# Kernel tuning notes

Hardware: AMD Instinct MI355X
Metric: run time of the kernel (lower is better)

The kernel has to match this reference:

```python
import jax, jax.numpy as jnp
import numpy as np

B_IN, B_MID, B_OUT = 30, 16, 10   # band widths: input sphere, after S2 conv, after SO3 conv
F1, F2 = 100, 100                 # feature channels
EPS = 1e-5


def _qw(b):
    """Driscoll-Healy quadrature weights over the 2b beta samples (SOFT grid)."""
    j = np.arange(2 * b)
    k = np.arange(b)
    s = (np.sin(np.pi * (2 * j[:, None] + 1) * (2 * k[None, :] + 1) / (4 * b))
         / (2 * k[None, :] + 1)).sum(1)
    return ((2.0 / b) * np.sin(np.pi * (2 * j + 1) / (4 * b)) * s).astype(np.float32)


def _wigner_d_all(l_max, betas):
    """Wigner-d matrices d^l(beta) = exp(-i beta Jy) in the |l,m> basis (m = -l..l).
    Returns list over l of real arrays [n_beta, 2l+1, 2l+1]."""
    betas = np.asarray(betas, np.float64)
    out = []
    for l in range(l_max):
        m = np.arange(-l, l + 1)
        dim = 2 * l + 1
        Jp = np.zeros((dim, dim))
        for i in range(dim - 1):
            Jp[i + 1, i] = np.sqrt(l * (l + 1) - m[i] * (m[i] + 1))
        Jy = (Jp - Jp.T) / 2j
        ev, V = np.linalg.eigh(Jy)
        ph = np.exp(-1j * betas[:, None] * ev[None, :])
        d = np.einsum('ak,bk,ck->bac', V, ph, V.conj())
        out.append(np.real(d).astype(np.float32))
    return out


def _project(x, b):
    """Radial max-projection of a point cloud [B,3,N] onto a (beta,alpha) grid -> [B,1,2b,2b]."""
    r = jnp.sqrt(jnp.sum(x * x, axis=1) + 1e-12)                       # [B,N]
    beta = jnp.arccos(jnp.clip(x[:, 2] / r, -1 + 1e-7, 1 - 1e-7))      # [0,pi]
    alpha = jnp.mod(jnp.arctan2(x[:, 1], x[:, 0]), 2 * np.pi)          # [0,2pi)
    jb = jnp.clip((beta / np.pi * (2 * b)).astype(jnp.int32), 0, 2 * b - 1)
    ja = jnp.clip((alpha / (2 * np.pi) * (2 * b)).astype(jnp.int32), 0, 2 * b - 1)
    flat = jb * (2 * b) + ja
    img = jax.vmap(lambda f, v: jnp.zeros((2 * b) ** 2, x.dtype).at[f].max(v))(flat, r)
    return img.reshape(x.shape[0], 1, 2 * b, 2 * b)


def _s2_fft(x, dm0_w):
    """x: [B,F,2b,2b] (beta,alpha) -> list over l of x_hat [B,F,2l+1] (complex)."""
    X = jnp.fft.fft(x, axis=-1)     # FFT over alpha
    n = x.shape[-1]
    hats = []
    for l, dw in enumerate(dm0_w):
        idx = np.mod(np.arange(-l, l + 1), n)
        hats.append(jnp.einsum('pm,BFpm->BFm', jnp.asarray(dw), X[..., idx]))
    return hats


def _so3_fft(x, dmn_w):
    """x: [B,F,2b,2b,2b] (beta,alpha,gamma) -> list over l of [B,F,2l+1,2l+1]."""
    X = jnp.fft.fftn(x, axes=(-2, -1))   # FFT over alpha, gamma
    n = x.shape[-1]
    hats = []
    for l, dw in enumerate(dmn_w):
        idx = np.mod(np.arange(-l, l + 1), n)
        Xl = X[:, :, :, idx[:, None], idx[None, :]]        # [B,F,2b,2l+1,2l+1]
        hats.append(jnp.einsum('pmn,BFpmn->BFmn', jnp.asarray(dw), Xl))
    return hats


def _so3_ifft(hats, b, d_list):
    """list over l of [B,F,2l+1,2l+1] -> real SO(3) signal [B,F,2b,2b,2b]."""
    Bb, Ff = hats[0].shape[:2]
    n = 2 * b
    Fg = jnp.zeros((Bb, Ff, n, n, n), jnp.complex64)   # (beta, m, n) freq grid
    for l, h in enumerate(hats):
        idx = np.mod(np.arange(-l, l + 1), n)
        c = (2 * l + 1) * jnp.einsum('pmn,BFmn->BFpmn', jnp.asarray(d_list[l]), h)
        Fg = Fg.at[:, :, :, idx[:, None], idx[None, :]].add(c)
    return jnp.real(jnp.fft.ifft2(Fg, axes=(-2, -1)))


def _bn_relu(x, g, b):
    mu = jnp.mean(x, axis=(0, 2, 3, 4), keepdims=True)
    var = jnp.var(x, axis=(0, 2, 3, 4), keepdims=True)
    xn = (x - mu) * jax.lax.rsqrt(var + EPS)
    return jax.nn.relu(xn * g[None, :, None, None, None] + b[None, :, None, None, None])


def _forward(x, w_s2, b_s2, bn1_gamma, bn1_beta, w_so3, b_so3, bn2_gamma, bn2_beta):
    # constant tables (numpy, computed eagerly)
    betas_in = (np.arange(2 * B_IN) + 0.5) * np.pi / (2 * B_IN)
    betas_mid = (np.arange(2 * B_MID) + 0.5) * np.pi / (2 * B_MID)
    betas_out = (np.arange(2 * B_OUT) + 0.5) * np.pi / (2 * B_OUT)
    w_in, w_mid, w_out = _qw(B_IN), _qw(B_MID), _qw(B_OUT)
    d_in = _wigner_d_all(B_MID, betas_in)
    d_mid = _wigner_d_all(B_MID, betas_mid)
    d_out = _wigner_d_all(B_OUT, betas_out)
    d_eq = _wigner_d_all(B_MID, np.array([np.pi / 2]))   # equatorial grid beta = pi/2

    img = _project(x, B_IN)                              # [B,1,60,60]

    # ---- S2 convolution: band 30 -> 16 ----
    dm0_w = [d_in[l][:, :, l] * w_in[:, None] for l in range(B_MID)]   # d^l_{m0} * quad weights
    xhat = _s2_fft(img, dm0_w)                           # list of [B,1,2l+1]
    k_s2 = w_s2.shape[-1]
    a_s2 = 2 * np.pi * np.arange(k_s2) / k_s2
    ws = w_s2 * np.float32(1.0 / np.sqrt(k_s2 * 1 * B_MID ** 4 / B_IN ** 2))
    zhat = []
    for l in range(B_MID):
        m = np.arange(-l, l + 1)
        sh = (d_eq[l][0][:, l][None, :] * np.exp(-1j * np.outer(a_s2, m))).astype(np.complex64)  # [k,m]
        yh = jnp.einsum('km,iok->mio', jnp.asarray(sh), ws)           # kernel spectrum [2l+1,f_in,f_out]
        zhat.append(jnp.einsum('Bim,nio->Bomn', xhat[l], jnp.conj(yh)))  # outer product m x n
    z = _so3_ifft(zhat, B_MID, d_mid) + b_s2[None, :, None, None, None]  # [B,100,32,32,32]
    z = _bn_relu(z, bn1_gamma, bn1_beta)

    # ---- SO3 convolution: band 16 -> 10 ----
    dmn_w = [d_mid[l] * w_mid[:, None, None] for l in range(B_OUT)]
    xhat2 = _so3_fft(z, dmn_w)                           # list of [B,100,2l+1,2l+1]
    k_so3 = w_so3.shape[-1]
    a_so3 = 2 * np.pi * np.arange(k_so3) / k_so3
    wk = w_so3 * np.float32(1.0 / np.sqrt(k_so3 * F1 * B_OUT ** 3 / B_MID ** 3))
    zhat2 = []
    for l in range(B_OUT):
        m = np.arange(-l, l + 1)
        U = (d_eq[l][0][None] * np.exp(-1j * np.outer(a_so3, m))[:, :, None]).astype(np.complex64)  # [k,m,n], gamma=0
        yh = jnp.einsum('kmn,iok->mnio', jnp.asarray(U), wk)
        zhat2.append(jnp.einsum('Bimk,nkio->Bomn', xhat2[l], jnp.conj(yh)))  # z^l = x^l y^l+
    z2 = _so3_ifft(zhat2, B_OUT, d_out) + b_so3[None, :, None, None, None]   # [B,100,20,20,20]
    z2 = _bn_relu(z2, bn2_gamma, bn2_beta)

    # ---- so3_integrate: sum over alpha/gamma, quadrature-weighted sum over beta ----
    return jnp.einsum('BCpag,p->BC', z2, jnp.asarray(w_out))   # [B,100]


def setup_inputs() -> dict:
    key = jax.random.key(0)
    k0, k1, k2 = jax.random.split(key, 3)
    B, N = 8, 2048
    return {
        "x": jax.random.normal(k0, (B, 3, N), jnp.float32),
        "w_s2": jax.random.normal(k1, (1, F1, 2 * B_IN), jnp.float32),
        "b_s2": jnp.zeros((F1,), jnp.float32),
        "bn1_gamma": jnp.ones((F1,), jnp.float32),
        "bn1_beta": jnp.zeros((F1,), jnp.float32),
        "w_so3": jax.random.normal(k2, (F1, F2, 2 * B_MID), jnp.float32),
        "b_so3": jnp.zeros((F2,), jnp.float32),
        "bn2_gamma": jnp.ones((F2,), jnp.float32),
        "bn2_beta": jnp.zeros((F2,), jnp.float32),
    }


def reference(x, w_s2, b_s2, bn1_gamma, bn1_beta, w_so3, b_so3, bn2_gamma, bn2_beta):
    return _forward(x, w_s2, b_s2, bn1_gamma, bn1_beta, w_so3, b_so3, bn2_gamma, bn2_beta)
```

## Files before the change

kernel.cpp:

```cpp
#include <hip/hip_runtime.h>
#include <math.h>

#define PI_D 3.14159265358979323846

constexpr int NBATCH = 8;
constexpr int NPTS   = 2048;
constexpr int F1C    = 100;
constexpr int F2C    = 100;

__host__ __device__ constexpr int S2c(int l){ return l*(2*l-1)*(2*l+1)/3; }

constexpr int OFF_WIN   = 0;
constexpr int OFF_WMID  = OFF_WIN + 60;
constexpr int OFF_WOUTQ = OFF_WMID + 32;
constexpr int OFF_DM0W  = OFF_WOUTQ + 20;
constexpr int OFF_DMID  = OFF_DM0W + 60*256;
constexpr int OFF_DOUT  = OFF_DMID + 32*S2c(16);
constexpr int OFF_DEQ   = OFF_DOUT + 20*S2c(10);
constexpr int OFF_IMG   = OFF_DEQ + S2c(16);
constexpr int OFF_XF    = OFF_IMG + NBATCH*60*60;
constexpr int OFF_XHAT  = OFF_XF + NBATCH*60*31*2;
constexpr int OFF_WS2   = OFF_XHAT + NBATCH*256*2;
constexpr int OFF_BN1   = OFF_WS2 + 100*31*2;
constexpr int OFF_BN1AB = OFF_BN1 + 200;
constexpr int OFF_BN2   = OFF_BN1AB + 200;
constexpr int OFF_BN2AB = OFF_BN2 + 200;
constexpr int OFF_LUTA  = OFF_BN2AB + 200;
constexpr int OFF_LUTB  = OFF_LUTA + 1330;
constexpr int OFF_LUTC  = OFF_LUTB + 1330;
constexpr int OFF_WCONV = OFF_LUTC + 1330;
constexpr int OFF_XHAT2 = OFF_WCONV + 100*100*19*2;
constexpr int OFF_SBUF  = OFF_XHAT2 + NBATCH*100*S2c(10)*2;
constexpr int OFF_ZHAT2 = OFF_SBUF + NBATCH*100*S2c(10)*2;
constexpr int OFF_Z2    = OFF_ZHAT2 + NBATCH*100*S2c(10)*2;
constexpr int OFF_Z     = OFF_Z2 + NBATCH*100*20*20*20;
constexpr int WS_TOTAL  = OFF_Z + NBATCH*100*32*32*32;
constexpr int OFF_HBUF  = OFF_Z2;

__device__ __forceinline__ int S2d(int l){ return l*(2*l-1)*(2*l+1)/3; }

__global__ void k_quad(float* ws){
  int j = threadIdx.x;
  if (j < 60){
    double bb = 30.0, s = 0.0;
    for (int k = 0; k < 30; ++k) s += sin(PI_D*(2*j+1)*(2*k+1)/(4.0*bb))/(2*k+1);
    ws[OFF_WIN+j] = (float)(2.0/bb * sin(PI_D*(2*j+1)/(4.0*bb)) * s);
  }
  if (j < 32){
    double bb = 16.0, s = 0.0;
    for (int k = 0; k < 16; ++k) s += sin(PI_D*(2*j+1)*(2*k+1)/(4.0*bb))/(2*k+1);
    ws[OFF_WMID+j] = (float)(2.0/bb * sin(PI_D*(2*j+1)/(4.0*bb)) * s);
  }
  if (j < 20){
    double bb = 10.0, s = 0.0;
    for (int k = 0; k < 10; ++k) s += sin(PI_D*(2*j+1)*(2*k+1)/(4.0*bb))/(2*k+1);
    ws[OFF_WOUTQ+j] = (float)(2.0/bb * sin(PI_D*(2*j+1)/(4.0*bb)) * s);
  }
}

__global__ void k_lut(float* ws){
  int q = blockIdx.x*blockDim.x + threadIdx.x;
  if (q >= 1330) return;
  int l = 0; while (S2d(l+1) <= q) ++l;
  int loc = q - S2d(l), tl = 2*l+1;
  int mm = loc/tl, nn = loc%tl;
  ((int*)(ws+OFF_LUTA))[q] = 32*S2d(l) + mm*tl + nn;
  ((int*)(ws+OFF_LUTB))[q] = ((mm-l+9)*19 + (nn-l+9)) | ((tl*tl) << 9) | ((nn-l+9) << 19);
  ((int*)(ws+OFF_LUTC))[q] = (S2d(l) + mm*tl) | ((S2d(l) + nn*tl) << 11) | (tl << 22);
}

__device__ double dev_wigner_t(const double* fact, int l, int mp, int m, double beta){
  double ch = cos(0.5*beta), sh = sin(0.5*beta);
  int kmin = m - mp; if (kmin < 0) kmin = 0;
  int kmax = l + m; if (l - mp < kmax) kmax = l - mp;
  double pref = sqrt(fact[l+mp]*fact[l-mp]*fact[l+m]*fact[l-m]);
  int ec = 2*l + m - mp - 2*kmin, es = mp - m + 2*kmin;
  double cp = 1.0, sp = 1.0;
  for (int e = 0; e < ec; ++e) cp *= ch;
  for (int e = 0; e < es; ++e) sp *= sh;
  double ch2i = 1.0/(ch*ch), sh2 = sh*sh;
  double sum = 0.0;
  for (int k = kmin; k <= kmax; ++k){
    double t = 1.0/(fact[l+m-k]*fact[k]*fact[l-mp-k]*fact[mp-m+k]);
    if ((mp-m+k) & 1) t = -t;
    sum += t*cp*sp;
    cp *= ch2i; sp *= sh2;
  }
  return pref*sum;
}

constexpr int N_DM0W = 60*256;
constexpr int N_DMID = 32*S2c(16);
constexpr int N_DOUT = 20*S2c(10);
constexpr int N_DEQ  = S2c(16);
constexpr int N_WIG  = N_DM0W + N_DMID + N_DOUT + N_DEQ;

__global__ void k_wigner(float* ws){
  __shared__ double fact[32];
  if (threadIdx.x == 0){ fact[0] = 1.0; for (int i = 1; i < 32; ++i) fact[i] = fact[i-1]*i; }
  __syncthreads();
  int idx = blockIdx.x*blockDim.x + threadIdx.x;
  if (idx >= N_WIG) return;
  if (idx < N_DM0W){
    int l = 0; while (60*(l+1)*(l+1) <= idx) ++l;
    int rem = idx - 60*l*l, tl = 2*l+1;
    int p = rem/tl, mm = rem%tl;
    double beta = (p+0.5)*PI_D/60.0;
    ws[OFF_DM0W+idx] = (float)dev_wigner_t(fact, l, mm-l, 0, beta) * ws[OFF_WIN+p];
    return;
  }
  idx -= N_DM0W;
  if (idx < N_DMID){
    int l = 0; while (32*S2d(l+1) <= idx) ++l;
    int rem = idx - 32*S2d(l), tl = 2*l+1;
    int q = rem % (tl*tl), p = rem/(tl*tl);
    int mm = q/tl, nn = q%tl;
    double beta = (p+0.5)*PI_D/32.0;
    ws[OFF_DMID+idx] = (float)dev_wigner_t(fact, l, mm-l, nn-l, beta);
    return;
  }
  idx -= N_DMID;
  if (idx < N_DOUT){
    int l = 0; while (20*S2d(l+1) <= idx) ++l;
    int rem = idx - 20*S2d(l), tl = 2*l+1;
    int q = rem % (tl*tl), p = rem/(tl*tl);
    int mm = q/tl, nn = q%tl;
    double beta = (p+0.5)*PI_D/20.0;
    ws[OFF_DOUT+idx] = (float)dev_wigner_t(fact, l, mm-l, nn-l, beta);
    return;
  }
  idx -= N_DOUT;
  {
    int l = 0; while (S2d(l+1) <= idx) ++l;
    int rem = idx - S2d(l), tl = 2*l+1;
    int mm = rem/tl, nn = rem%tl;
    ws[OFF_DEQ+idx] = (float)dev_wigner_t(fact, l, mm-l, nn-l, 0.5*PI_D);
  }
}

__global__ void k_project(const float* __restrict__ x, float* ws){
  int t = blockIdx.x*blockDim.x + threadIdx.x;
  if (t >= NBATCH*NPTS) return;
  int b = t / NPTS, n = t % NPTS;
  const float* xb = x + (size_t)b*3*NPTS;
  float xx = xb[n], yy = xb[NPTS+n], zz = xb[2*NPTS+n];
  float r = sqrtf(xx*xx + yy*yy + zz*zz + 1e-12f);
  float ct = zz / r;
  ct = fminf(fmaxf(ct, -1.0f + 1e-7f), 1.0f - 1e-7f);
  float beta = acosf(ct);
  float alpha = atan2f(yy, xx);
  if (alpha < 0.0f) alpha += 2.0f*(float)PI_D;
  int jb = (int)((beta / (float)PI_D) * 60.0f);
  jb = jb < 0 ? 0 : (jb > 59 ? 59 : jb);
  int ja = (int)((alpha / (2.0f*(float)PI_D)) * 60.0f);
  ja = ja < 0 ? 0 : (ja > 59 ? 59 : ja);
  unsigned* img = (unsigned*)(ws + OFF_IMG) + (b*3600 + jb*60 + ja);
  atomicMax(img, __float_as_uint(r));
}

__global__ void k_s2dft(float* ws){
  int t = blockIdx.x*blockDim.x + threadIdx.x;
  if (t >= NBATCH*60*31) return;
  int b = t/(60*31), r = t%(60*31);
  int p = r/31, mi = r%31, m = mi - 15;
  const float* img = ws + OFF_IMG + (b*60 + p)*60;
  float sr = 0.f, si = 0.f;
  for (int a = 0; a < 60; ++a){
    int k = ((a*m) % 60 + 60) % 60;
    float c = cospif(k/30.0f), s = sinpif(k/30.0f);
    float v = img[a];
    sr += v*c; si -= v*s;
  }
  ws[OFF_XF + t*2]   = sr;
  ws[OFF_XF + t*2+1] = si;
}

__global__ void k_xhat(float* ws){
  int t = blockIdx.x*blockDim.x + threadIdx.x;
  if (t >= NBATCH*256) return;
  int b = t/256, flat = t%256;
  int l = 0; while ((l+1)*(l+1) <= flat) ++l;
  int mm = flat - l*l, tl = 2*l+1;
  int mi = mm - l + 15;
  float sr = 0.f, si = 0.f;
  for (int p = 0; p < 60; ++p){
    float w = ws[OFF_DM0W + 60*l*l + p*tl + mm];
    sr += w * ws[OFF_XF + ((b*60+p)*31 + mi)*2];
    si += w * ws[OFF_XF + ((b*60+p)*31 + mi)*2 + 1];
  }
  ws[OFF_XHAT + t*2]   = sr;
  ws[OFF_XHAT + t*2+1] = si;
}

__global__ void k_ws2(float* ws, const float* __restrict__ w_s2, float scale1){
  int t = blockIdx.x*blockDim.x + threadIdx.x;
  if (t >= 100*31) return;
  int o = t/31, ni = t%31, n = ni - 15;
  float sr = 0.f, si = 0.f;
  for (int k = 0; k < 60; ++k){
    int kk = ((k*n) % 60 + 60) % 60;
    float c = cospif(kk/30.0f), s = sinpif(kk/30.0f);
    float v = w_s2[o*60 + k] * scale1;
    sr += v*c; si += v*s;
  }
  ws[OFF_WS2 + t*2]   = sr;
  ws[OFF_WS2 + t*2+1] = si;
}

__global__ __launch_bounds__(256) void k_H(float* ws){
  int bid = blockIdx.x;
  int p = bid & 31, b = bid >> 5;
  __shared__ float xh[512], Dt[256];
  __shared__ int dbase[16];
  int tid = threadIdx.x;
  {
    int flat = tid;
    int l = 0; while ((l+1)*(l+1) <= flat) ++l;
    int mm = flat - l*l, tl = 2*l+1;
    xh[2*flat]   = ws[OFF_XHAT + (b*256+flat)*2];
    xh[2*flat+1] = ws[OFF_XHAT + (b*256+flat)*2+1];
    Dt[flat] = (float)tl * ws[OFF_DEQ + S2d(l) + mm*tl + l];
  }
  if (tid < 16){ int l = tid, tl = 2*l+1; dbase[l] = OFF_DMID + 32*S2d(l) + p*tl*tl; }
  __syncthreads();
  float* Hb = ws + OFF_HBUF + (size_t)bid*992;
  for (int q = tid; q < 496; q += 256){
    int m = q/31, ni = q%31, n = ni-15;
    int an = n < 0 ? -n : n;
    int lmin = m > an ? m : an;
    float ar = 0.f, ai = 0.f;
    for (int l = lmin; l < 16; ++l){
      int tl = 2*l+1;
      float d = ws[dbase[l] + (m+l)*tl + (n+l)];
      float t = d * Dt[l*l + (n+l)];
      int fa = l*l + (m+l);
      ar += t*xh[2*fa]; ai += t*xh[2*fa+1];
    }
    Hb[2*q] = ar; Hb[2*q+1] = ai;
  }
}

__global__ __launch_bounds__(256) void k_so3ifft_mid(float* ws, const float* __restrict__ b_s2){
  int bid = blockIdx.x;
  int p = bid & 31, bo = bid >> 5;
  int o = bo % F1C, b = bo / F1C;
  __shared__ float Fg[992], tmpS[1024];
  __shared__ float twr[32], twi[32], Wr[31], Wi[31], redA[4], redB[4];
  int tid = threadIdx.x;
  if (tid < 32){ twr[tid] = cospif(tid/16.0f); twi[tid] = sinpif(tid/16.0f); }
  if (tid < 31){ Wr[tid] = ws[OFF_WS2 + (o*31+tid)*2]; Wi[tid] = ws[OFF_WS2 + (o*31+tid)*2+1]; }
  __syncthreads();
  {
    const float* Hb = ws + OFF_HBUF + (size_t)((b<<5)|p)*992;
    for (int q = tid; q < 496; q += 256){
      int ni = q % 31;
      float hr = Hb[2*q], hi = Hb[2*q+1];
      float wr = Wr[ni], wi = Wi[ni];
      Fg[2*q]   = hr*wr - hi*wi;
      Fg[2*q+1] = hr*wi + hi*wr;
    }
  }
  __syncthreads();
  if (tid < 128){
    int m = tid >> 3, g0 = tid & 7;
    float T0r=0,T0i=0,T1r=0,T1i=0,T2r=0,T2i=0,T3r=0,T3i=0;
    int base = 2*m*31;
    #pragma unroll
    for (int ni = 0; ni < 31; ++ni){
      int k = ((ni-15)*g0) & 31;
      float c = twr[k], s = twi[k];
      float fr = Fg[base+2*ni], fi = Fg[base+2*ni+1];
      float re = fr*c - fi*s, im = fr*s + fi*c;
      int cc = (ni+1) & 3;
      if (cc == 0){ T0r += re; T0i += im; }
      else if (cc == 1){ T1r += re; T1i += im; }
      else if (cc == 2){ T2r += re; T2i += im; }
      else { T3r += re; T3i += im; }
    }
    float Ar=T0r+T2r, Ai=T0i+T2i, Br=T0r-T2r, Bi=T0i-T2i;
    float Cr=T1r+T3r, Ci=T1i+T3i, Dr=T1r-T3r, Di=T1i-T3i;
    int ix = 2*(m*32+g0);
    tmpS[ix]      = Ar+Cr; tmpS[ix+1]    = Ai+Ci;
    tmpS[ix+16]   = Br-Di; tmpS[ix+17]   = Bi+Dr;
    tmpS[ix+32]   = Ar-Cr; tmpS[ix+33]   = Ai-Ci;
    tmpS[ix+48]   = Br+Di; tmpS[ix+49]   = Bi-Dr;
  }
  __syncthreads();
  float bsv = b_s2[o];
  float lsum = 0.f, lss = 0.f;
  float* z = ws + OFF_Z;
  size_t zb = ((size_t)(b*F1C+o)*32 + p)*1024;
  {
    int a0 = tid >> 5, g = tid & 31;
    float U0r=0, U2r=0, U1r=0, U1i=0, U3r=0, U3i=0;
    #pragma unroll
    for (int m = 1; m < 16; ++m){
      int k = (m*a0) & 31;
      float c = twr[k], s = twi[k];
      float tr = tmpS[2*(m*32+g)], ti = tmpS[2*(m*32+g)+1];
      float re = tr*c - ti*s;
      int cc = m & 3;
      if (cc == 0) U0r += re;
      else if (cc == 2) U2r += re;
      else {
        float im = tr*s + ti*c;
        if (cc == 1){ U1r += re; U1i += im; }
        else        { U3r += re; U3i += im; }
      }
    }
    float Ar = U0r + U2r, Br = U0r - U2r;
    float Cr = U1r + U3r, Di = U1i - U3i;
    float t0 = tmpS[2*g];
    float v0 = (t0 + 2.0f*(Ar + Cr))*(1.0f/1024.0f) + bsv;
    float v1 = (t0 + 2.0f*(Br - Di))*(1.0f/1024.0f) + bsv;
    float v2 = (t0 + 2.0f*(Ar - Cr))*(1.0f/1024.0f) + bsv;
    float v3 = (t0 + 2.0f*(Br + Di))*(1.0f/1024.0f) + bsv;
    z[zb + (a0     )*32 + g] = v0;
    z[zb + (a0 +  8)*32 + g] = v1;
    z[zb + (a0 + 16)*32 + g] = v2;
    z[zb + (a0 + 24)*32 + g] = v3;
    lsum = v0+v1+v2+v3;
    lss  = v0*v0+v1*v1+v2*v2+v3*v3;
  }
  for (int off = 32; off; off >>= 1){ lsum += __shfl_down(lsum, off); lss += __shfl_down(lss, off); }
  if ((tid & 63) == 0){ redA[tid>>6] = lsum; redB[tid>>6] = lss; }
  __syncthreads();
  if (tid == 0){
    atomicAdd(&ws[OFF_BN1 + o],       redA[0]+redA[1]+redA[2]+redA[3]);
    atomicAdd(&ws[OFF_BN1 + 100 + o], redB[0]+redB[1]+redB[2]+redB[3]);
  }
}

__global__ void k_bnfin1(float* ws, const float* __restrict__ g1, const float* __restrict__ be1){
  int t = threadIdx.x;
  if (t >= 100) return;
  const float invN = 1.0f/262144.0f;
  float mu = ws[OFF_BN1+t]*invN;
  float var = ws[OFF_BN1+100+t]*invN - mu*mu;
  float sA = rsqrtf(var + 1e-5f) * g1[t];
  ws[OFF_BN1AB+t]     = sA;
  ws[OFF_BN1AB+100+t] = be1[t] - mu*sA;
}

__global__ __launch_bounds__(256) void k_so3fft_a(float* ws){
  int bid = blockIdx.x;
  int p = bid & 31, bo = bid >> 5;
  int o = bo % F1C;
  __shared__ float y[32*33];
  __shared__ float Bs[32*36];
  __shared__ float t1[1216];
  __shared__ float twr[32], twi[32];
  int tid = threadIdx.x;
  if (tid < 32){ twr[tid] = cospif(tid/16.0f); twi[tid] = sinpif(tid/16.0f); }
  float sA = ws[OFF_BN1AB+o], sB = ws[OFF_BN1AB+100+o];
  float* zp = ws + OFF_Z + (size_t)bid*1024;
  for (int q = tid; q < 1024; q += 256){
    float v = zp[q]*sA + sB;
    y[(q>>5)*33 + (q&31)] = v > 0.f ? v : 0.f;
  }
  __syncthreads();
  {
    int a = tid >> 3, g2 = tid & 7;
    float y0 = y[a*33+g2], y1 = y[a*33+g2+8], y2 = y[a*33+g2+16], y3 = y[a*33+g2+24];
    float e = y0+y2, f = y1+y3;
    int bb = a*36 + g2*4;
    Bs[bb]   = e+f;
    Bs[bb+1] = e-f;
    Bs[bb+2] = y0-y2;
    Bs[bb+3] = -(y1-y3);
  }
  __syncthreads();
  for (int q = tid; q < 320; q += 256){
    int a = q/10, n = q%10, ni = 9+n;
    int c = n & 3;
    int bb = a*36;
    float sr = 0.f, si = 0.f;
    if ((c & 1) == 0){
      int off = bb + (c >> 1);
      #pragma unroll
      for (int g2 = 0; g2 < 8; ++g2){
        int k = (g2*n) & 31;
        float B = Bs[off + g2*4];
        sr += B*twr[k]; si -= B*twi[k];
      }
    } else {
      float sgn = (c == 1) ? 1.f : -1.f;
      #pragma unroll
      for (int g2 = 0; g2 < 8; ++g2){
        int k = (g2*n) & 31;
        float cc_ = twr[k], ss = twi[k];
        float br = Bs[bb+g2*4+2], bi = sgn*Bs[bb+g2*4+3];
        sr += br*cc_ + bi*ss;
        si += bi*cc_ - br*ss;
      }
    }
    t1[2*(a*19+ni)] = sr; t1[2*(a*19+ni)+1] = si;
  }
  __syncthreads();
  for (int q = tid; q < 160; q += 256){
    int a = q/10, ni = 9 + q%10;
    int i0 = 2*(a*19+ni), i1 = 2*((a+16)*19+ni);
    float xr=t1[i0], xi=t1[i0+1], yr=t1[i1], yi=t1[i1+1];
    t1[i0]=xr+yr; t1[i0+1]=xi+yi; t1[i1]=xr-yr; t1[i1+1]=xi-yi;
  }
  __syncthreads();
  float wm = ws[OFF_WMID+p];
  for (int q = tid; q < 190; q += 256){
    int m = q/10 - 9, nio = q%10, ni = 9+nio;
    int off = (m & 1) ? 16*19 : 0;
    float sr = 0.f, si = 0.f;
    for (int a = 0; a < 16; ++a){
      int k = (a*m) & 31;
      float c = twr[k], s = twi[k];
      float tr = t1[2*(off+a*19+ni)], ti = t1[2*(off+a*19+ni)+1];
      sr += tr*c + ti*s;
      si += ti*c - tr*s;
    }
    sr *= wm; si *= wm;
    int qf = (m+9)*19 + ni;
    zp[2*qf] = sr; zp[2*qf+1] = si;
    if (nio > 0){
      int qm = (9-m)*19 + (9-nio);
      zp[2*qm] = sr; zp[2*qm+1] = -si;
    }
  }
}

__global__ __launch_bounds__(512) void k_so3fft_b(float* ws){
  int bo = blockIdx.x;
  int tid = threadIdx.x;
  __shared__ float xw[722];
  __shared__ float xh2[2660];
  const float* xwbase = ws + OFF_Z + (size_t)bo*32*1024;
  const int* lutA = (const int*)(ws + OFF_LUTA);
  const int* lutB = (const int*)(ws + OFF_LUTB);
  const int* lutC = (const int*)(ws + OFF_LUTC);
  float accr[3], acci[3];
  int la[3], xi2[3], tl2v[3];
  #pragma unroll
  for (int j = 0; j < 3; ++j){
    accr[j] = 0.f; acci[j] = 0.f;
    int q = tid + 512*j;
    if (q < 1330){ la[j] = lutA[q]; int lb = lutB[q]; xi2[j] = 2*(lb & 511); tl2v[j] = (lb >> 9) & 1023; }
    else { la[j] = 0; xi2[j] = 0; tl2v[j] = 0; }
  }
  for (int pp = 0; pp < 32; ++pp){
    __syncthreads();
    for (int u = tid; u < 722; u += 512) xw[u] = xwbase[pp*1024 + u];
    __syncthreads();
    #pragma unroll
    for (int j = 0; j < 3; ++j){
      int q = tid + 512*j;
      if (q < 1330){
        float d = ws[OFF_DMID + la[j] + pp*tl2v[j]];
        accr[j] += d*xw[xi2[j]]; acci[j] += d*xw[xi2[j]+1];
      }
    }
  }
  #pragma unroll
  for (int j = 0; j < 3; ++j){
    int q = tid + 512*j;
    if (q < 1330){ xh2[2*q] = accr[j]; xh2[2*q+1] = acci[j]; }
  }
  __syncthreads();
  #pragma unroll
  for (int j = 0; j < 3; ++j){
    int q = tid + 512*j;
    if (q < 1330){
      int lc = lutC[q];
      int rowstart = lc & 2047, deqrow = (lc >> 11) & 2047, tl = lc >> 22;
      const float* dq = ws + OFF_DEQ + deqrow;
      const float* xb = xh2 + 2*rowstart;
      float sr = 0.f, si = 0.f;
      for (int k = 0; k < tl; ++k){
        float d = dq[k];
        sr += d*xb[2*k]; si += d*xb[2*k+1];
      }
      int base = OFF_SBUF + (bo*1330 + q)*2;
      ws[base]   = sr;
      ws[base+1] = si;
    }
  }
}

__global__ void k_wconv(float* ws, const float* __restrict__ w_so3, float scale2){
  int t = blockIdx.x*blockDim.x + threadIdx.x;
  if (t >= 100*100*19) return;
  int ni = t % 19, io = t / 19;
  int n = ni - 9;
  float sr = 0.f, si = 0.f;
  for (int j = 0; j < 32; ++j){
    int k = (j*n) & 31;
    float c = cospif(k/16.0f), s = sinpif(k/16.0f);
    float v = w_so3[io*32 + j] * scale2;
    sr += v*c; si += v*s;
  }
  ws[OFF_WCONV + t*2]   = sr;
  ws[OFF_WCONV + t*2+1] = si;
}

__global__ void k_zhat2(float* ws){
  int t = blockIdx.x*blockDim.x + threadIdx.x;
  if (t >= NBATCH*50*1330) return;
  int q = t % 1330, boo = t / 1330;
  int oq = boo % 50, b = boo / 50;
  int o0 = oq*2;
  int lb = ((const int*)(ws+OFF_LUTB))[q];
  int ni = (lb >> 19) & 31;
  const float* sp  = ws + OFF_SBUF + (size_t)(b*100)*2660 + 2*q;
  const float* wp0 = ws + OFF_WCONV + (size_t)(o0*19 + ni)*2;
  const float* wp1 = wp0 + 38;
  float sr0 = 0.f, si0 = 0.f, sr1 = 0.f, si1 = 0.f;
  for (int i = 0; i < 100; ++i){
    float Sr = sp[0], Si = sp[1];
    float W0r = wp0[0], W0i = wp0[1];
    float W1r = wp1[0], W1i = wp1[1];
    sr0 += Sr*W0r - Si*W0i;
    si0 += Sr*W0i + Si*W0r;
    sr1 += Sr*W1r - Si*W1i;
    si1 += Sr*W1i + Si*W1r;
    sp += 2660;
    wp0 += 3800;
    wp1 += 3800;
  }
  size_t zb0 = ((size_t)(b*100 + o0)*1330 + q)*2;
  ws[OFF_ZHAT2 + zb0]          = sr0;
  ws[OFF_ZHAT2 + zb0 + 1]      = si0;
  ws[OFF_ZHAT2 + zb0 + 2660]   = sr1;
  ws[OFF_ZHAT2 + zb0 + 2661]   = si1;
}

__global__ __launch_bounds__(256) void k_so3ifft_out(float* ws, const float* __restrict__ b_so3){
  int bid = blockIdx.x;
  int pg = bid % 5, bo = bid / 5;
  int o = bo % F2C, b = bo / F2C;
  __shared__ __align__(16) float zh[2660];
  __shared__ float Fg[380], tmpS[400];
  __shared__ float twr[20], twi[20], redA[4], redB[4];
  int tid = threadIdx.x;
  {
    const float4* zsrc = (const float4*)(ws + OFF_ZHAT2 + (size_t)bo*2660);
    float4* zds = (float4*)zh;
    for (int q = tid; q < 665; q += 256) zds[q] = zsrc[q];
  }
  if (tid < 20){ twr[tid] = cospif(tid/10.0f); twi[tid] = sinpif(tid/10.0f); }
  __syncthreads();
  float bsv = b_so3[o];
  float lsum = 0.f, lss = 0.f;
  float* z2 = ws + OFF_Z2;
  for (int pp = 0; pp < 4; ++pp){
    int p = pg*4 + pp;
    for (int q = tid; q < 190; q += 256){
      int m = q/19, ni = q%19, n = ni-9;
      int an = n < 0 ? -n : n;
      int lmin = m > an ? m : an;
      float ar = 0.f, ai = 0.f;
      for (int l = lmin; l < 10; ++l){
        int tl = 2*l+1;
        float d = ws[OFF_DOUT + 20*S2d(l) + (p*tl + (m+l))*tl + (n+l)] * (float)tl;
        int fz = S2d(l) + (m+l)*tl + (n+l);
        ar += d*zh[2*fz]; ai += d*zh[2*fz+1];
      }
      Fg[2*q] = ar; Fg[2*q+1] = ai;
    }
    __syncthreads();
    for (int q = tid; q < 100; q += 256){
      int m = q/10, g = q%10;
      float Er=0.f, Ei=0.f, Or=0.f, Oi=0.f;
      int base = 2*m*19;
      for (int ni = 1; ni < 19; ni += 2){
        int n = ni-9;
        int k = ((n*g) % 20 + 20) % 20;
        float c = twr[k], s = twi[k];
        float fr = Fg[base+2*ni], fi = Fg[base+2*ni+1];
        Er += fr*c - fi*s; Ei += fr*s + fi*c;
      }
      for (int ni = 0; ni < 19; ni += 2){
        int n = ni-9;
        int k = ((n*g) % 20 + 20) % 20;
        float c = twr[k], s = twi[k];
        float fr = Fg[base+2*ni], fi = Fg[base+2*ni+1];
        Or += fr*c - fi*s; Oi += fr*s + fi*c;
      }
      tmpS[2*(m*20+g)]      = Er+Or; tmpS[2*(m*20+g)+1]      = Ei+Oi;
      tmpS[2*(m*20+g+10)]   = Er-Or; tmpS[2*(m*20+g+10)+1]   = Ei-Oi;
    }
    __syncthreads();
    size_t zb = ((size_t)bo*20 + p)*400;
    for (int q = tid; q < 200; q += 256){
      int a = q/20, g = q%20;
      float E = 0.f, O = 0.f;
      for (int m = 2; m < 10; m += 2){
        int k = (m*a) % 20;
        E += tmpS[2*(m*20+g)]*twr[k] - tmpS[2*(m*20+g)+1]*twi[k];
      }
      for (int m = 1; m < 10; m += 2){
        int k = (m*a) % 20;
        O += tmpS[2*(m*20+g)]*twr[k] - tmpS[2*(m*20+g)+1]*twi[k];
      }
      float t0 = tmpS[2*g];
      float v1 = (t0 + 2.0f*(E+O))*(1.0f/400.0f) + bsv;
      float v2 = (t0 + 2.0f*(E-O))*(1.0f/400.0f) + bsv;
      z2[zb + a*20 + g]       = v1;
      z2[zb + (a+10)*20 + g]  = v2;
      lsum += v1+v2; lss += v1*v1+v2*v2;
    }
    __syncthreads();
  }
  for (int off = 32; off; off >>= 1){ lsum += __shfl_down(lsum, off); lss += __shfl_down(lss, off); }
  if ((tid & 63) == 0){ redA[tid>>6] = lsum; redB[tid>>6] = lss; }
  __syncthreads();
  if (tid == 0){
    atomicAdd(&ws[OFF_BN2 + o],       redA[0]+redA[1]+redA[2]+redA[3]);
    atomicAdd(&ws[OFF_BN2 + 100 + o], redB[0]+redB[1]+redB[2]+redB[3]);
  }
}

__global__ void k_bnfin2(float* ws, const float* __restrict__ g2, const float* __restrict__ be2){
  int t = threadIdx.x;
  if (t >= 100) return;
  const float invN = 1.0f/64000.0f;
  float mu = ws[OFF_BN2+t]*invN;
  float var = ws[OFF_BN2+100+t]*invN - mu*mu;
  float sA = rsqrtf(var + 1e-5f) * g2[t];
  ws[OFF_BN2AB+t]     = sA;
  ws[OFF_BN2AB+100+t] = be2[t] - mu*sA;
}

__global__ __launch_bounds__(256) void k_final(float* ws, float* __restrict__ out){
  int bid = blockIdx.x;
  int c = bid % 100, b = bid / 100;
  int tid = threadIdx.x;
  float sA = ws[OFF_BN2AB+c], sB = ws[OFF_BN2AB+100+c];
  const float* z2 = ws + OFF_Z2 + (size_t)(b*100+c)*8000;
  float lsum = 0.f;
  for (int q = tid; q < 8000; q += 256){
    int p = q / 400;
    float v = z2[q]*sA + sB;
    v = v > 0.f ? v : 0.f;
    lsum += v * ws[OFF_WOUTQ + p];
  }
  for (int off = 32; off; off >>= 1) lsum += __shfl_down(lsum, off);
  __shared__ float red[4];
  if ((tid & 63) == 0) red[tid>>6] = lsum;
  __syncthreads();
  if (tid == 0) out[b*100 + c] = red[0]+red[1]+red[2]+red[3];
}

extern "C" void kernel_launch(void* const* d_in, const int* in_sizes, int n_in,
                              void* d_out, int out_size, void* d_ws, size_t ws_size,
                              hipStream_t stream){
  const float* x      = (const float*)d_in[0];
  const float* w_s2   = (const float*)d_in[1];
  const float* b_s2   = (const float*)d_in[2];
  const float* g1     = (const float*)d_in[3];
  const float* be1    = (const float*)d_in[4];
  const float* w_so3  = (const float*)d_in[5];
  const float* b_so3  = (const float*)d_in[6];
  const float* g2     = (const float*)d_in[7];
  const float* be2    = (const float*)d_in[8];
  float* ws  = (float*)d_ws;
  float* out = (float*)d_out;

  hipMemsetAsync(ws + OFF_IMG, 0, NBATCH*3600*sizeof(float), stream);
  hipMemsetAsync(ws + OFF_BN1, 0, 200*sizeof(float), stream);
  hipMemsetAsync(ws + OFF_BN2, 0, 200*sizeof(float), stream);

  k_quad<<<1, 128, 0, stream>>>(ws);
  k_lut<<<6, 256, 0, stream>>>(ws);
  k_wigner<<<(N_WIG + 255)/256, 256, 0, stream>>>(ws);
  k_project<<<(NBATCH*NPTS + 255)/256, 256, 0, stream>>>(x, ws);
  k_s2dft<<<(NBATCH*60*31 + 255)/256, 256, 0, stream>>>(ws);
  k_xhat<<<(NBATCH*256 + 255)/256, 256, 0, stream>>>(ws);
  float scale1 = (float)(1.0/sqrt(60.0*1.0*65536.0/900.0));
  k_ws2<<<(100*31 + 255)/256, 256, 0, stream>>>(ws, w_s2, scale1);
  k_H<<<NBATCH*32, 256, 0, stream>>>(ws);
  k_so3ifft_mid<<<NBATCH*F1C*32, 256, 0, stream>>>(ws, b_s2);
  k_bnfin1<<<1, 128, 0, stream>>>(ws, g1, be1);
  k_so3fft_a<<<NBATCH*F1C*32, 256, 0, stream>>>(ws);
  k_so3fft_b<<<NBATCH*F1C, 512, 0, stream>>>(ws);
  float scale2 = (float)(1.0/sqrt(32.0*100.0*1000.0/4096.0));
  k_wconv<<<(100*100*19 + 255)/256, 256, 0, stream>>>(ws, w_so3, scale2);
  k_zhat2<<<(NBATCH*50*1330 + 255)/256, 256, 0, stream>>>(ws);
  k_so3ifft_out<<<NBATCH*F2C*5, 256, 0, stream>>>(ws, b_so3);
  k_bnfin2<<<1, 128, 0, stream>>>(ws, g2, be2);
  k_final<<<NBATCH*100, 256, 0, stream>>>(ws, out);
}
```

Baseline: 498.0 us.

## Drop quadrature kernel, vectorize loads, widen zhat2 outputs, rebalance ifft blocks

Removes the separate quadrature-weight launch by folding the mid and output weights into k_lut and recomputing the input weights inline in k_wigner. The BN+ReLU loads in k_so3fft_a and k_final now use float4. k_zhat2 computes four output channels per thread instead of two, so each S load is reused more. k_so3ifft_out uses 4 blocks of 5 beta slices instead of 5 blocks of 4. The aim is fewer launches and less memory traffic, at the cost of redundant double-precision trig in k_wigner and higher register pressure in k_zhat2.

```diff
diff --git a/kernel.cpp b/kernel.cpp
--- a/kernel.cpp
+++ b/kernel.cpp
@@ -39,27 +39,18 @@
 
 __device__ __forceinline__ int S2d(int l){ return l*(2*l-1)*(2*l+1)/3; }
 
-__global__ void k_quad(float* ws){
-  int j = threadIdx.x;
-  if (j < 60){
-    double bb = 30.0, s = 0.0;
-    for (int k = 0; k < 30; ++k) s += sin(PI_D*(2*j+1)*(2*k+1)/(4.0*bb))/(2*k+1);
-    ws[OFF_WIN+j] = (float)(2.0/bb * sin(PI_D*(2*j+1)/(4.0*bb)) * s);
-  }
-  if (j < 32){
+__global__ void k_lut(float* ws){
+  int q = blockIdx.x*blockDim.x + threadIdx.x;
+  if (q < 32){
     double bb = 16.0, s = 0.0;
-    for (int k = 0; k < 16; ++k) s += sin(PI_D*(2*j+1)*(2*k+1)/(4.0*bb))/(2*k+1);
-    ws[OFF_WMID+j] = (float)(2.0/bb * sin(PI_D*(2*j+1)/(4.0*bb)) * s);
-  }
-  if (j < 20){
+    for (int k = 0; k < 16; ++k) s += sin(PI_D*(2*q+1)*(2*k+1)/(4.0*bb))/(2*k+1);
+    ws[OFF_WMID+q] = (float)(2.0/bb * sin(PI_D*(2*q+1)/(4.0*bb)) * s);
+  } else if (q < 52){
+    int j = q - 32;
     double bb = 10.0, s = 0.0;
     for (int k = 0; k < 10; ++k) s += sin(PI_D*(2*j+1)*(2*k+1)/(4.0*bb))/(2*k+1);
     ws[OFF_WOUTQ+j] = (float)(2.0/bb * sin(PI_D*(2*j+1)/(4.0*bb)) * s);
   }
-}
-
-__global__ void k_lut(float* ws){
-  int q = blockIdx.x*blockDim.x + threadIdx.x;
   if (q >= 1330) return;
   int l = 0; while (S2d(l+1) <= q) ++l;
   int loc = q - S2d(l), tl = 2*l+1;
@@ -106,7 +97,10 @@
     int rem = idx - 60*l*l, tl = 2*l+1;
     int p = rem/tl, mm = rem%tl;
     double beta = (p+0.5)*PI_D/60.0;
-    ws[OFF_DM0W+idx] = (float)dev_wigner_t(fact, l, mm-l, 0, beta) * ws[OFF_WIN+p];
+    double s = 0.0;
+    for (int k = 0; k < 30; ++k) s += sin(PI_D*(2*p+1)*(2*k+1)/120.0)/(2*k+1);
+    double w_in = (2.0/30.0) * sin(PI_D*(2*p+1)/120.0) * s;
+    ws[OFF_DM0W+idx] = (float)(dev_wigner_t(fact, l, mm-l, 0, beta) * w_in);
     return;
   }
   idx -= N_DM0W;
@@ -354,9 +348,16 @@
   if (tid < 32){ twr[tid] = cospif(tid/16.0f); twi[tid] = sinpif(tid/16.0f); }
   float sA = ws[OFF_BN1AB+o], sB = ws[OFF_BN1AB+100+o];
   float* zp = ws + OFF_Z + (size_t)bid*1024;
-  for (int q = tid; q < 1024; q += 256){
-    float v = zp[q]*sA + sB;
-    y[(q>>5)*33 + (q&31)] = v > 0.f ? v : 0.f;
+  {
+    const float4* z4 = (const float4*)zp;
+    float4 v = z4[tid];
+    int a = tid >> 3, g4 = (tid & 7)*4;
+    float* yr = y + a*33 + g4;
+    float t0 = v.x*sA + sB, t1v = v.y*sA + sB, t2 = v.z*sA + sB, t3 = v.w*sA + sB;
+    yr[0] = t0 > 0.f ? t0 : 0.f;
+    yr[1] = t1v > 0.f ? t1v : 0.f;
+    yr[2] = t2 > 0.f ? t2 : 0.f;
+    yr[3] = t3 > 0.f ? t3 : 0.f;
   }
   __syncthreads();
   {
@@ -501,38 +502,41 @@
 
 __global__ void k_zhat2(float* ws){
   int t = blockIdx.x*blockDim.x + threadIdx.x;
-  if (t >= NBATCH*50*1330) return;
+  if (t >= NBATCH*25*1330) return;
   int q = t % 1330, boo = t / 1330;
-  int oq = boo % 50, b = boo / 50;
-  int o0 = oq*2;
+  int oq = boo % 25, b = boo / 25;
+  int o0 = oq*4;
   int lb = ((const int*)(ws+OFF_LUTB))[q];
   int ni = (lb >> 19) & 31;
   const float* sp  = ws + OFF_SBUF + (size_t)(b*100)*2660 + 2*q;
   const float* wp0 = ws + OFF_WCONV + (size_t)(o0*19 + ni)*2;
   const float* wp1 = wp0 + 38;
-  float sr0 = 0.f, si0 = 0.f, sr1 = 0.f, si1 = 0.f;
+  const float* wp2 = wp0 + 76;
+  const float* wp3 = wp0 + 114;
+  float sr0=0,si0=0,sr1=0,si1=0,sr2=0,si2=0,sr3=0,si3=0;
   for (int i = 0; i < 100; ++i){
     float Sr = sp[0], Si = sp[1];
     float W0r = wp0[0], W0i = wp0[1];
     float W1r = wp1[0], W1i = wp1[1];
-    sr0 += Sr*W0r - Si*W0i;
-    si0 += Sr*W0i + Si*W0r;
-    sr1 += Sr*W1r - Si*W1i;
-    si1 += Sr*W1i + Si*W1r;
+    float W2r = wp2[0], W2i = wp2[1];
+    float W3r = wp3[0], W3i = wp3[1];
+    sr0 += Sr*W0r - Si*W0i; si0 += Sr*W0i + Si*W0r;
+    sr1 += Sr*W1r - Si*W1i; si1 += Sr*W1i + Si*W1r;
+    sr2 += Sr*W2r - Si*W2i; si2 += Sr*W2i + Si*W2r;
+    sr3 += Sr*W3r - Si*W3i; si3 += Sr*W3i + Si*W3r;
     sp += 2660;
-    wp0 += 3800;
-    wp1 += 3800;
-  }
-  size_t zb0 = ((size_t)(b*100 + o0)*1330 + q)*2;
-  ws[OFF_ZHAT2 + zb0]          = sr0;
-  ws[OFF_ZHAT2 + zb0 + 1]      = si0;
-  ws[OFF_ZHAT2 + zb0 + 2660]   = sr1;
-  ws[OFF_ZHAT2 + zb0 + 2661]   = si1;
+    wp0 += 3800; wp1 += 3800; wp2 += 3800; wp3 += 3800;
+  }
+  size_t zb0 = (size_t)OFF_ZHAT2 + ((size_t)(b*100 + o0)*1330 + q)*2;
+  ws[zb0]          = sr0; ws[zb0 + 1]      = si0;
+  ws[zb0 + 2660]   = sr1; ws[zb0 + 2661]   = si1;
+  ws[zb0 + 5320]   = sr2; ws[zb0 + 5321]   = si2;
+  ws[zb0 + 7980]   = sr3; ws[zb0 + 7981]   = si3;
 }
 
 __global__ __launch_bounds__(256) void k_so3ifft_out(float* ws, const float* __restrict__ b_so3){
   int bid = blockIdx.x;
-  int pg = bid % 5, bo = bid / 5;
+  int pg = bid % 4, bo = bid / 4;
   int o = bo % F2C, b = bo / F2C;
   __shared__ __align__(16) float zh[2660];
   __shared__ float Fg[380], tmpS[400];
@@ -548,8 +552,8 @@
   float bsv = b_so3[o];
   float lsum = 0.f, lss = 0.f;
   float* z2 = ws + OFF_Z2;
-  for (int pp = 0; pp < 4; ++pp){
-    int p = pg*4 + pp;
+  for (int pp = 0; pp < 5; ++pp){
+    int p = pg*5 + pp;
     for (int q = tid; q < 190; q += 256){
       int m = q/19, ni = q%19, n = ni-9;
       int an = n < 0 ? -n : n;
@@ -632,13 +636,18 @@
   int c = bid % 100, b = bid / 100;
   int tid = threadIdx.x;
   float sA = ws[OFF_BN2AB+c], sB = ws[OFF_BN2AB+100+c];
-  const float* z2 = ws + OFF_Z2 + (size_t)(b*100+c)*8000;
+  const float4* z2 = (const float4*)(ws + OFF_Z2 + (size_t)(b*100+c)*8000);
   float lsum = 0.f;
-  for (int q = tid; q < 8000; q += 256){
-    int p = q / 400;
-    float v = z2[q]*sA + sB;
-    v = v > 0.f ? v : 0.f;
-    lsum += v * ws[OFF_WOUTQ + p];
+  for (int j = tid; j < 2000; j += 256){
+    int p = j / 100;
+    float wq = ws[OFF_WOUTQ + p];
+    float4 v = z2[j];
+    float t0 = v.x*sA + sB, t1 = v.y*sA + sB, t2 = v.z*sA + sB, t3 = v.w*sA + sB;
+    t0 = t0 > 0.f ? t0 : 0.f;
+    t1 = t1 > 0.f ? t1 : 0.f;
+    t2 = t2 > 0.f ? t2 : 0.f;
+    t3 = t3 > 0.f ? t3 : 0.f;
+    lsum += (t0+t1+t2+t3) * wq;
   }
   for (int off = 32; off; off >>= 1) lsum += __shfl_down(lsum, off);
   __shared__ float red[4];
@@ -666,7 +675,6 @@
   hipMemsetAsync(ws + OFF_BN1, 0, 200*sizeof(float), stream);
   hipMemsetAsync(ws + OFF_BN2, 0, 200*sizeof(float), stream);
 
-  k_quad<<<1, 128, 0, stream>>>(ws);
   k_lut<<<6, 256, 0, stream>>>(ws);
   k_wigner<<<(N_WIG + 255)/256, 256, 0, stream>>>(ws);
   k_project<<<(NBATCH*NPTS + 255)/256, 256, 0, stream>>>(x, ws);
@@ -681,8 +689,8 @@
   k_so3fft_b<<<NBATCH*F1C, 512, 0, stream>>>(ws);
   float scale2 = (float)(1.0/sqrt(32.0*100.0*1000.0/4096.0));
   k_wconv<<<(100*100*19 + 255)/256, 256, 0, stream>>>(ws, w_so3, scale2);
-  k_zhat2<<<(NBATCH*50*1330 + 255)/256, 256, 0, stream>>>(ws);
-  k_so3ifft_out<<<NBATCH*F2C*5, 256, 0, stream>>>(ws, b_so3);
+  k_zhat2<<<(NBATCH*25*1330 + 255)/256, 256, 0, stream>>>(ws);
+  k_so3ifft_out<<<NBATCH*F2C*4, 256, 0, stream>>>(ws, b_so3);
   k_bnfin2<<<1, 128, 0, stream>>>(ws, g2, be2);
   k_final<<<NBATCH*100, 256, 0, stream>>>(ws, out);
 }
```

Result: faster. 479.7 us (-3.7%).
